# Kernel optimization log

Measured on AMD Instinct MI355X. Metric: run time of the kernel, lower is better.

## Reference

```python
import jax, jax.numpy as jnp
import numpy as np
import math

D_MODEL = 1024
N_HEADS = 16
D_FF = 4096
B, T = 2, 2048
EPS = 1e-5


def setup_inputs() -> dict:
    key = jax.random.key(0)
    ks = jax.random.split(key, 8)
    s = 0.02
    return {
        "x": jax.random.normal(ks[0], (B, T, D_MODEL), jnp.float32),
        "wq": jax.random.normal(ks[1], (D_MODEL, D_MODEL), jnp.float32) * s,
        "wk": jax.random.normal(ks[2], (D_MODEL, D_MODEL), jnp.float32) * s,
        "wv": jax.random.normal(ks[3], (D_MODEL, D_MODEL), jnp.float32) * s,
        "wo": jax.random.normal(ks[4], (D_MODEL, D_MODEL), jnp.float32) * s,
        "ln1_w": jnp.ones((D_MODEL,), jnp.float32),
        "ln2_w": jnp.ones((D_MODEL,), jnp.float32),
        "w1": jax.random.normal(ks[5], (D_FF, D_MODEL), jnp.float32) * s,
        "w2": jax.random.normal(ks[6], (D_MODEL, D_FF), jnp.float32) * s,
    }


def rmsnorm(x, w):
    # weight * x / sqrt(mean(x^2) + eps)
    denom = jnp.sqrt(jnp.mean(jnp.square(x), axis=-1, keepdims=True) + EPS)
    return w * x / denom


def mhsa(x, wq, wk, wv, wo):
    b, t, d = x.shape
    dk = d // N_HEADS
    # Linear(weight shape (out,in)): y = x @ W.T
    q = (x @ wq.T).reshape(b, t, N_HEADS, dk).transpose(0, 2, 1, 3)  # bhtd
    k = (x @ wk.T).reshape(b, t, N_HEADS, dk).transpose(0, 2, 1, 3)
    v = (x @ wv.T).reshape(b, t, N_HEADS, dk).transpose(0, 2, 1, 3)
    scores = jnp.einsum("bhqd,bhkd->bhqk", q, k) / math.sqrt(dk)
    causal = jnp.tril(jnp.ones((t, t), bool))  # True = keep
    scores = jnp.where(causal, scores, -jnp.inf)
    probs = jax.nn.softmax(scores, axis=-1)
    out = jnp.einsum("bhqk,bhkd->bhqd", probs, v)
    out = out.transpose(0, 2, 1, 3).reshape(b, t, d)
    return out @ wo.T


def ffn(x, w1, w2):
    h = jax.nn.gelu(x @ w1.T, approximate=False)  # exact erf GELU
    return h @ w2.T


def reference(x, wq, wk, wv, wo, ln1_w, ln2_w, w1, w2):
    x = x + mhsa(rmsnorm(x, ln1_w), wq, wk, wv, wo)
    x = x + ffn(rmsnorm(x, ln2_w), w1, w2)
    return x
```

## Files before the change

### kernel.cpp

```cpp
#include <hip/hip_runtime.h>
#include <stdint.h>

#define D_MODEL 1024
#define N_HEADS 16
#define D_FF    4096
#define BATCH   2
#define SEQ     2048
#define EPSV    1e-5f
#define MTOK    (BATCH*SEQ)
#define QKVS    3072


typedef __bf16 bf16x8 __attribute__((ext_vector_type(8)));
typedef float  f32x4  __attribute__((ext_vector_type(4)));

#define MFMA_BF16(a,b,c) __builtin_amdgcn_mfma_f32_16x16x32_bf16((a),(b),(c),0,0,0)

__device__ __forceinline__ float b2f(unsigned short u) {
  union { unsigned int i; float f; } c; c.i = ((unsigned int)u) << 16; return c.f;
}
__device__ __forceinline__ unsigned short f2b(float f) {
  union { float f; unsigned int i; } c; c.f = f;
  unsigned int x = c.i;
  unsigned int r = (x + 0x7fffu + ((x >> 16) & 1u)) >> 16;
  return (unsigned short)r;
}
__device__ __forceinline__ unsigned short f2b_trunc(float f) {
  union { float f; unsigned int i; } c; c.f = f;
  return (unsigned short)(c.i >> 16);
}

__device__ __forceinline__ void glds16(const unsigned short* g, unsigned short* l) {
  __builtin_amdgcn_global_load_lds(
      (const __attribute__((address_space(1))) void*)g,
      (__attribute__((address_space(3))) void*)l, 16, 0, 0);
}

__global__ void detect_kernel(const unsigned int* __restrict__ ln1, int* __restrict__ flag) {
  if (threadIdx.x == 0 && blockIdx.x == 0)
    *flag = (ln1[0] == 0x3F800000u) ? 1 : 0;
}

__global__ void convert_all_kernel(
    const void* __restrict__ wq, const void* __restrict__ wk,
    const void* __restrict__ wv, const void* __restrict__ wo,
    const void* __restrict__ w1, const void* __restrict__ w2,
    const void* __restrict__ l1, const void* __restrict__ l2,
    unsigned short* dq, unsigned short* dk, unsigned short* dv, unsigned short* dwo,
    unsigned short* d1, unsigned short* d2, unsigned short* dl1, unsigned short* dl2,
    const int* __restrict__ flag) {
  const int i = blockIdx.x * 256 + threadIdx.x;
  const void* src; unsigned short* dst; int off;
  if (i < 1048576) {
    const int t = i >> 18;  off = i & 262143;
    src = (t == 0) ? wq : (t == 1) ? wk : (t == 2) ? wv : wo;
    dst = (t == 0) ? dq : (t == 1) ? dk : (t == 2) ? dv : dwo;
  } else if (i < 2097152) { off = i - 1048576; src = w1; dst = d1; }
  else if (i < 3145728)   { off = i - 2097152; src = w2; dst = d2; }
  else if (i < 3145984)   { off = i - 3145728; src = l1; dst = dl1; }
  else                    { off = i - 3145984; src = l2; dst = dl2; }
  if (*flag) {
    const float4 v = ((const float4*)src)[off];
    ushort4 o; o.x = f2b(v.x); o.y = f2b(v.y); o.z = f2b(v.z); o.w = f2b(v.w);
    ((ushort4*)dst)[off] = o;
  } else {
    ((ushort4*)dst)[off] = ((const ushort4*)src)[off];
  }
}

__global__ void rmsnorm_kernel(const void* __restrict__ xin,
                               const unsigned short* __restrict__ w,
                               unsigned short* __restrict__ out,
                               const int* __restrict__ f32flag) {
  __shared__ float red[4];
  const int row = blockIdx.x;
  const int tid = threadIdx.x;
  const int base = tid * 4;
  const bool f32 = f32flag && (*f32flag != 0);
  float v0, v1, v2, v3;
  if (f32) {
    const float4 p = ((const float4*)xin)[(size_t)row * 256 + tid];
    v0 = p.x; v1 = p.y; v2 = p.z; v3 = p.w;
  } else {
    const short4 p = *(const short4*)((const unsigned short*)xin + (size_t)row * D_MODEL + base);
    v0 = b2f((unsigned short)p.x); v1 = b2f((unsigned short)p.y);
    v2 = b2f((unsigned short)p.z); v3 = b2f((unsigned short)p.w);
  }
  float ss = v0*v0 + v1*v1 + v2*v2 + v3*v3;
  #pragma unroll
  for (int d = 1; d < 64; d <<= 1) ss += __shfl_xor(ss, d);
  if ((tid & 63) == 0) red[tid >> 6] = ss;
  __syncthreads();
  const float tot = red[0] + red[1] + red[2] + red[3];
  const float inv = 1.0f / sqrtf(tot * (1.0f / (float)D_MODEL) + EPSV);
  short4 ov;
  ov.x = (short)f2b(b2f(w[base + 0]) * v0 * inv);
  ov.y = (short)f2b(b2f(w[base + 1]) * v1 * inv);
  ov.z = (short)f2b(b2f(w[base + 2]) * v2 * inv);
  ov.w = (short)f2b(b2f(w[base + 3]) * v3 * inv);
  *(short4*)(out + (size_t)row * D_MODEL + base) = ov;
}

#define BM 128
#define BK 32
template<int TBN>
__global__ __launch_bounds__(256) void gemm_bt_kernel(
    const unsigned short* __restrict__ A,
    const unsigned short* __restrict__ Bw,
    void* __restrict__ C,
    const void* __restrict__ R,
    int M, int N, int K, int flags,
    const int* __restrict__ outf32_flag,
    const int* __restrict__ resf32_flag) {
  constexpr int JN = TBN / 32;
  constexpr int GA = BM * 4;
  constexpr int GT = (BM + TBN) * 4;
  __shared__ __align__(16) unsigned short As[BM * BK];
  __shared__ __align__(16) unsigned short Bs[TBN * BK];

  const int tid  = threadIdx.x;
  const int w    = tid >> 6, ln = tid & 63;
  const int wm   = w >> 1,  wn = w & 1;
  const int lm   = ln & 15, quad = ln >> 4;

  const int gx = gridDim.x;
  const int L  = blockIdx.x + gx * blockIdx.y;
  const int per = (gx * gridDim.y) >> 3;
  const int tile = (L & 7) * per + (L >> 3);
  const int tileM = (tile / gx) * BM;
  const int tileN = (tile % gx) * TBN;

  f32x4 acc[4][JN];
  #pragma unroll
  for (int i = 0; i < 4; i++)
    #pragma unroll
    for (int j = 0; j < JN; j++) acc[i][j] = (f32x4){0.f, 0.f, 0.f, 0.f};

  for (int k0 = 0; k0 < K; k0 += BK) {
    __syncthreads();
    #pragma unroll
    for (int g0 = 0; g0 < GT; g0 += 256) {
      const int g = g0 + tid;
      if (g0 + 256 <= GA || g < GA) {
        const int r  = g >> 2;
        const int sg = (g & 3) ^ ((g >> 3) & 3);
        glds16(&A[(size_t)(tileM + r) * K + k0 + sg * 8], &As[g * 8]);
      } else {
        const int gb = g - GA;
        const int r  = gb >> 2;
        const int sg = (gb & 3) ^ ((gb >> 3) & 3);
        glds16(&Bw[(size_t)(tileN + r) * K + k0 + sg * 8], &Bs[gb * 8]);
      }
    }
    __syncthreads();

    bf16x8 af[4], bfr[JN];
    #pragma unroll
    for (int i = 0; i < 4; i++) {
      const int r = wm * 64 + i * 16 + lm;
      af[i] = *(const bf16x8*)&As[r * BK + (quad ^ ((r >> 1) & 3)) * 8];
    }
    #pragma unroll
    for (int j = 0; j < JN; j++) {
      const int r = wn * (TBN / 2) + j * 16 + lm;
      bfr[j] = *(const bf16x8*)&Bs[r * BK + (quad ^ ((r >> 1) & 3)) * 8];
    }
    #pragma unroll
    for (int i = 0; i < 4; i++)
      #pragma unroll
      for (int j = 0; j < JN; j++)
        acc[i][j] = MFMA_BF16(af[i], bfr[j], acc[i][j]);
  }

  const bool hasR   = flags & 2;
  const bool dogelu = flags & 8;
  const bool outf32 = outf32_flag && (*outf32_flag != 0);
  const bool rf32   = resf32_flag && (*resf32_flag != 0);
  #pragma unroll
  for (int i = 0; i < 4; i++) {
    #pragma unroll
    for (int j = 0; j < JN; j++) {
      #pragma unroll
      for (int r = 0; r < 4; r++) {
        const int row = tileM + wm * 64 + i * 16 + quad * 4 + r;
        const int col = tileN + wn * (TBN / 2) + j * 16 + lm;
        float val = acc[i][j][r];
        if (dogelu) {
          const float u = 0.7978845608f * (val + 0.044715f * val * val * val);
          const float e = exp2f(u * 2.885390082f);
          val = 0.5f * val * (2.0f - 2.0f / (e + 1.0f));
        }
        const size_t idx = (size_t)row * N + col;
        if (hasR) val += rf32 ? ((const float*)R)[idx]
                              : b2f(((const unsigned short*)R)[idx]);
        if (outf32) ((float*)C)[idx] = val;
        else        ((unsigned short*)C)[idx] = f2b(val);
      }
    }
  }
}

__global__ __launch_bounds__(256) void attn_kernel(
    const unsigned short* __restrict__ QKV,
    unsigned short* __restrict__ O) {
  __shared__ __align__(16) unsigned short Ks [2][64 * 64];
  __shared__ __align__(16) unsigned short VTs[2][64 * 64];
  __shared__ __align__(16) unsigned short Ps [4][16 * 64];

  const int tid = threadIdx.x;
  const int w = tid >> 6, ln = tid & 63;
  const int lm = ln & 15, quad = ln >> 4;
  const f32x4 zf = (f32x4){0.f, 0.f, 0.f, 0.f};

  const int L   = blockIdx.x;
  const int xcd = L & 7;
  const int idx = L >> 3;
  const int bh  = xcd * 4 + (idx >> 4);
  const int pr  = idx & 15;
  const int b   = bh >> 4, h = bh & 15;
  const int qtA = pr, qtB = 31 - pr;
  const int nA = qtA + 1, total = nA + qtB + 1;

  const unsigned short* Qp = QKV + (size_t)b * SEQ * QKVS + h * 64;
  const unsigned short* Kp = Qp + 1024;
  const unsigned short* Vp = Qp + 2048;

  auto scale8 = [](bf16x8 v) -> bf16x8 {
    union { bf16x8 h; unsigned short u[8]; } in, out;
    in.h = v;
    #pragma unroll
    for (int ii = 0; ii < 8; ii++) out.u[ii] = f2b(b2f(in.u[ii]) * 0.1803368801f);
    return out.h;
  };

  bf16x8 qfA0, qfA1, qfB0, qfB1;
  {
    const size_t ra = (size_t)(qtA * 64 + w * 16 + lm) * QKVS;
    qfA0 = scale8(*(const bf16x8*)&Qp[ra + quad * 8]);
    qfA1 = scale8(*(const bf16x8*)&Qp[ra + 32 + quad * 8]);
    const size_t rb = (size_t)(qtB * 64 + w * 16 + lm) * QKVS;
    qfB0 = scale8(*(const bf16x8*)&Qp[rb + quad * 8]);
    qfB1 = scale8(*(const bf16x8*)&Qp[rb + 32 + quad * 8]);
  }

  const int vkey2 = (tid >> 3) << 1;
  const int vd8   = (tid & 7) << 3;
  const int ve    = tid & 7;

  f32x4 oacc[4];
  float lrow[4];
  #pragma unroll
  for (int i = 0; i < 4; i++) oacc[i] = zf;
  #pragma unroll
  for (int r = 0; r < 4; r++) lrow[r] = 0.f;

  union V8 { uint4 u; unsigned short s[8]; };
  V8 v0r, v1r;

  auto issue_stage = [&](int c, int buf) {
    #pragma unroll
    for (int ii = 0; ii < 2; ii++) {
      const int g   = tid + 256 * ii;
      const int key = g >> 3;
      const int sg  = (g & 7) ^ (key & 7);
      glds16(&Kp[(size_t)(c * 64 + key) * QKVS + sg * 8], &Ks[buf][g * 8]);
    }
    v0r.u = *(const uint4*)&Vp[(size_t)(c * 64 + vkey2)     * QKVS + vd8];
    v1r.u = *(const uint4*)&Vp[(size_t)(c * 64 + vkey2 + 1) * QKVS + vd8];
  };

  auto write_vt = [&](int buf) {
    const int swb = (vkey2 >> 3) ^ ve;
    #pragma unroll
    for (int ii = 0; ii < 8; ii++) {
      const int phys = (vd8 + ii) * 64 + swb * 8 + (vkey2 & 7);
      const unsigned int pk = (unsigned int)v0r.s[ii] | ((unsigned int)v1r.s[ii] << 16);
      *(unsigned int*)&VTs[buf][phys] = pk;
    }
  };

  auto write_o = [&](int qt) {
    #pragma unroll
    for (int r = 0; r < 4; r++) {
      float l = lrow[r];
      #pragma unroll
      for (int d2 = 1; d2 < 16; d2 <<= 1) l += __shfl_xor(l, d2);
      const float invl = 1.0f / l;
      const size_t orow = (size_t)(b * SEQ + qt * 64 + w * 16 + quad * 4 + r) * D_MODEL + h * 64;
      #pragma unroll
      for (int nt = 0; nt < 4; nt++)
        O[orow + nt * 16 + lm] = f2b(oacc[nt][r] * invl);
    }
  };

  issue_stage(0, 0);
  for (int j = 0; j < total; j++) {
    const int buf = j & 1;
    write_vt(buf);
    __syncthreads();

    if (j + 1 < total) {
      const int cn = (j + 1 < nA) ? (j + 1) : (j + 1 - nA);
      issue_stage(cn, buf ^ 1);
    }
    if (j == nA) {
      write_o(qtA);
      #pragma unroll
      for (int i = 0; i < 4; i++) oacc[i] = zf;
      #pragma unroll
      for (int r = 0; r < 4; r++) lrow[r] = 0.f;
    }

    const bool isA = j < nA;
    const int  c   = isA ? j : j - nA;
    const int  qt  = isA ? qtA : qtB;
    const bool diag = (c == qt);
    const bf16x8 qf0 = isA ? qfA0 : qfB0;
    const bf16x8 qf1 = isA ? qfA1 : qfB1;

    f32x4 s[4];
    #pragma unroll
    for (int kg = 0; kg < 4; kg++) {
      const int kbase = (kg * 16 + lm) * 64;
      const int s0 = quad ^ (lm & 7);
      const bf16x8 kf0 = *(const bf16x8*)&Ks[buf][kbase + s0 * 8];
      const bf16x8 kf1 = *(const bf16x8*)&Ks[buf][kbase + (s0 ^ 4) * 8];
      s[kg] = MFMA_BF16(qf0, kf0, zf);
      s[kg] = MFMA_BF16(qf1, kf1, s[kg]);
    }

    #pragma unroll
    for (int r = 0; r < 4; r++) {
      float a0 = s[0][r], a1 = s[1][r], a2 = s[2][r], a3 = s[3][r];
      if (diag) {
        const int qloc = w * 16 + quad * 4 + r;
        if (lm      > qloc) a0 = -1e30f;
        if (lm + 16 > qloc) a1 = -1e30f;
        if (lm + 32 > qloc) a2 = -1e30f;
        if (lm + 48 > qloc) a3 = -1e30f;
      }
      const float p0 = exp2f(a0), p1 = exp2f(a1);
      const float p2 = exp2f(a2), p3 = exp2f(a3);
      lrow[r] += (p0 + p1) + (p2 + p3);
      const int row = quad * 4 + r;
      const int rb  = row * 64, r7 = row & 7, lhi = lm >> 3, llo = lm & 7;
      Ps[w][rb + (((0 + lhi) ^ r7) << 3) + llo] = f2b_trunc(p0);
      Ps[w][rb + (((2 + lhi) ^ r7) << 3) + llo] = f2b_trunc(p1);
      Ps[w][rb + (((4 + lhi) ^ r7) << 3) + llo] = f2b_trunc(p2);
      Ps[w][rb + (((6 + lhi) ^ r7) << 3) + llo] = f2b_trunc(p3);
    }

    #pragma unroll
    for (int hh = 0; hh < 2; hh++) {
      const bf16x8 pf = *(const bf16x8*)&Ps[w][lm * 64 + (((hh * 4 + quad) ^ (lm & 7)) << 3)];
      #pragma unroll
      for (int nt = 0; nt < 4; nt++) {
        const int dim = nt * 16 + lm;
        const int swb = (hh * 4 + quad) ^ (dim >> 3);
        const bf16x8 vf = *(const bf16x8*)&VTs[buf][dim * 64 + swb * 8];
        oacc[nt] = MFMA_BF16(pf, vf, oacc[nt]);
      }
    }
  }
  write_o(qtB);
}

extern "C" void kernel_launch(void* const* d_in, const int* in_sizes, int n_in,
                              void* d_out, int out_size, void* d_ws, size_t ws_size,
                              hipStream_t stream) {
  char* ws = (char*)d_ws;
  const size_t MB = 1u << 20;
  unsigned short* cwq  = (unsigned short*)(ws + 8  * MB);
  unsigned short* cwk  = (unsigned short*)(ws + 10 * MB);
  unsigned short* cwv  = (unsigned short*)(ws + 12 * MB);
  unsigned short* cwo  = (unsigned short*)(ws + 14 * MB);
  unsigned short* cln1 = (unsigned short*)(ws + 16 * MB);
  unsigned short* cln2 = (unsigned short*)(ws + 16 * MB + 4096);
  unsigned short* cw1  = (unsigned short*)(ws + 17 * MB);
  unsigned short* cw2  = (unsigned short*)(ws + 25 * MB);
  unsigned short* xn1  = (unsigned short*)(ws + 33 * MB);
  unsigned short* qkv  = (unsigned short*)(ws + 41 * MB);
  unsigned short* y1   = (unsigned short*)(ws + 65 * MB);
  unsigned short* xn2  = (unsigned short*)(ws + 0);
  unsigned short* hbf  = (unsigned short*)(ws + 33 * MB);
  int*            flag = (int*)           (ws + 73 * MB);
  unsigned short* ao   = xn1;

  detect_kernel<<<1, 64, 0, stream>>>((const unsigned int*)d_in[5], flag);

  convert_all_kernel<<<12290, 256, 0, stream>>>(
      d_in[1], d_in[2], d_in[3], d_in[4], d_in[7], d_in[8], d_in[5], d_in[6],
      cwq, cwk, cwv, cwo, cw1, cw2, cln1, cln2, flag);

  rmsnorm_kernel<<<MTOK, 256, 0, stream>>>(d_in[0], cln1, xn1, flag);
  {
    const dim3 g(QKVS / 128, MTOK / BM);
    gemm_bt_kernel<128><<<g, 256, 0, stream>>>(xn1, cwq, qkv, nullptr,
                                               MTOK, QKVS, D_MODEL, 0, nullptr, nullptr);
  }
  attn_kernel<<<512, 256, 0, stream>>>(qkv, ao);
  {
    const dim3 g(D_MODEL / 64, MTOK / BM);
    gemm_bt_kernel<64><<<g, 256, 0, stream>>>(ao, cwo, y1, d_in[0],
                                              MTOK, D_MODEL, D_MODEL, 2, nullptr, flag);
  }
  rmsnorm_kernel<<<MTOK, 256, 0, stream>>>(y1, cln2, xn2, nullptr);
  {
    const dim3 g(D_FF / 128, MTOK / BM);
    gemm_bt_kernel<128><<<g, 256, 0, stream>>>(xn2, cw1, hbf, nullptr,
                                               MTOK, D_FF, D_MODEL, 8, nullptr, nullptr);
  }
  {
    const dim3 g(D_MODEL / 64, MTOK / BM);
    gemm_bt_kernel<64><<<g, 256, 0, stream>>>(hbf, cw2, d_out, y1,
                                              MTOK, D_MODEL, D_FF, 2, flag, nullptr);
  }
}
```

Before: 402.3 us.

## Split K across two warp groups in narrow GEMMs with LDS reduction

```diff
diff --git a/kernel.cpp b/kernel.cpp
--- a/kernel.cpp
+++ b/kernel.cpp
@@ -103,8 +103,8 @@
 
 #define BM 128
 #define BK 32
-template<int TBN>
-__global__ __launch_bounds__(256) void gemm_bt_kernel(
+template<int TBN, int KSEG>
+__global__ __launch_bounds__(256 * KSEG) void gemm_bt_kernel(
     const unsigned short* __restrict__ A,
     const unsigned short* __restrict__ Bw,
     void* __restrict__ C,
@@ -115,13 +115,19 @@
   constexpr int JN = TBN / 32;
   constexpr int GA = BM * 4;
   constexpr int GT = (BM + TBN) * 4;
-  __shared__ __align__(16) unsigned short As[BM * BK];
-  __shared__ __align__(16) unsigned short Bs[TBN * BK];
-
-  const int tid  = threadIdx.x;
-  const int w    = tid >> 6, ln = tid & 63;
-  const int wm   = w >> 1,  wn = w & 1;
-  const int lm   = ln & 15, quad = ln >> 4;
+  __shared__ __align__(16) unsigned short smem[KSEG * (BM + TBN) * BK];
+  unsigned short* Asb = smem;
+  unsigned short* Bsb = smem + KSEG * BM * BK;
+
+  const int tid   = threadIdx.x;
+  const int tid_l = tid & 255;
+  const int w     = tid >> 6;
+  const int kseg  = (KSEG == 1) ? 0 : (w >> 2);
+  const int wm    = (w >> 1) & 1, wn = w & 1;
+  const int ln    = tid & 63;
+  const int lm    = ln & 15, quad = ln >> 4;
+  unsigned short* As = Asb + kseg * BM * BK;
+  unsigned short* Bs = Bsb + kseg * TBN * BK;
 
   const int gx = gridDim.x;
   const int L  = blockIdx.x + gx * blockIdx.y;
@@ -130,26 +136,28 @@
   const int tileM = (tile / gx) * BM;
   const int tileN = (tile % gx) * TBN;
 
+  const int kofs = kseg * (K / KSEG);
+
   f32x4 acc[4][JN];
   #pragma unroll
   for (int i = 0; i < 4; i++)
     #pragma unroll
     for (int j = 0; j < JN; j++) acc[i][j] = (f32x4){0.f, 0.f, 0.f, 0.f};
 
-  for (int k0 = 0; k0 < K; k0 += BK) {
+  for (int k0 = 0; k0 < K / KSEG; k0 += BK) {
     __syncthreads();
     #pragma unroll
     for (int g0 = 0; g0 < GT; g0 += 256) {
-      const int g = g0 + tid;
+      const int g = g0 + tid_l;
       if (g0 + 256 <= GA || g < GA) {
         const int r  = g >> 2;
         const int sg = (g & 3) ^ ((g >> 3) & 3);
-        glds16(&A[(size_t)(tileM + r) * K + k0 + sg * 8], &As[g * 8]);
+        glds16(&A[(size_t)(tileM + r) * K + kofs + k0 + sg * 8], &As[g * 8]);
       } else {
         const int gb = g - GA;
         const int r  = gb >> 2;
         const int sg = (gb & 3) ^ ((gb >> 3) & 3);
-        glds16(&Bw[(size_t)(tileN + r) * K + k0 + sg * 8], &Bs[gb * 8]);
+        glds16(&Bw[(size_t)(tileN + r) * K + kofs + k0 + sg * 8], &Bs[gb * 8]);
       }
     }
     __syncthreads();
@@ -172,29 +180,54 @@
         acc[i][j] = MFMA_BF16(af[i], bfr[j], acc[i][j]);
   }
 
-  const bool hasR   = flags & 2;
-  const bool dogelu = flags & 8;
-  const bool outf32 = outf32_flag && (*outf32_flag != 0);
-  const bool rf32   = resf32_flag && (*resf32_flag != 0);
-  #pragma unroll
-  for (int i = 0; i < 4; i++) {
+  if constexpr (KSEG == 2) {
+    float* scratch = (float*)smem;
     #pragma unroll
     for (int j = 0; j < JN; j++) {
-      #pragma unroll
-      for (int r = 0; r < 4; r++) {
-        const int row = tileM + wm * 64 + i * 16 + quad * 4 + r;
-        const int col = tileN + wn * (TBN / 2) + j * 16 + lm;
-        float val = acc[i][j][r];
-        if (dogelu) {
-          const float u = 0.7978845608f * (val + 0.044715f * val * val * val);
-          const float e = exp2f(u * 2.885390082f);
-          val = 0.5f * val * (2.0f - 2.0f / (e + 1.0f));
+      __syncthreads();
+      if (kseg == 1) {
+        #pragma unroll
+        for (int i = 0; i < 4; i++)
+          #pragma unroll
+          for (int r = 0; r < 4; r++)
+            scratch[tid_l * 16 + i * 4 + r] = acc[i][j][r];
+      }
+      __syncthreads();
+      if (kseg == 0) {
+        #pragma unroll
+        for (int i = 0; i < 4; i++)
+          #pragma unroll
+          for (int r = 0; r < 4; r++)
+            acc[i][j][r] += scratch[tid_l * 16 + i * 4 + r];
+      }
+    }
+  }
+
+  if (kseg == 0) {
+    const bool hasR   = flags & 2;
+    const bool dogelu = flags & 8;
+    const bool outf32 = outf32_flag && (*outf32_flag != 0);
+    const bool rf32   = resf32_flag && (*resf32_flag != 0);
+    #pragma unroll
+    for (int i = 0; i < 4; i++) {
+      #pragma unroll
+      for (int j = 0; j < JN; j++) {
+        #pragma unroll
+        for (int r = 0; r < 4; r++) {
+          const int row = tileM + wm * 64 + i * 16 + quad * 4 + r;
+          const int col = tileN + wn * (TBN / 2) + j * 16 + lm;
+          float val = acc[i][j][r];
+          if (dogelu) {
+            const float u = 0.7978845608f * (val + 0.044715f * val * val * val);
+            const float e = exp2f(u * 2.885390082f);
+            val = 0.5f * val * (2.0f - 2.0f / (e + 1.0f));
+          }
+          const size_t idx = (size_t)row * N + col;
+          if (hasR) val += rf32 ? ((const float*)R)[idx]
+                                : b2f(((const unsigned short*)R)[idx]);
+          if (outf32) ((float*)C)[idx] = val;
+          else        ((unsigned short*)C)[idx] = f2b(val);
         }
-        const size_t idx = (size_t)row * N + col;
-        if (hasR) val += rf32 ? ((const float*)R)[idx]
-                              : b2f(((const unsigned short*)R)[idx]);
-        if (outf32) ((float*)C)[idx] = val;
-        else        ((unsigned short*)C)[idx] = f2b(val);
       }
     }
   }
@@ -395,24 +428,24 @@
   rmsnorm_kernel<<<MTOK, 256, 0, stream>>>(d_in[0], cln1, xn1, flag);
   {
     const dim3 g(QKVS / 128, MTOK / BM);
-    gemm_bt_kernel<128><<<g, 256, 0, stream>>>(xn1, cwq, qkv, nullptr,
-                                               MTOK, QKVS, D_MODEL, 0, nullptr, nullptr);
+    gemm_bt_kernel<128,1><<<g, 256, 0, stream>>>(xn1, cwq, qkv, nullptr,
+                                                 MTOK, QKVS, D_MODEL, 0, nullptr, nullptr);
   }
   attn_kernel<<<512, 256, 0, stream>>>(qkv, ao);
   {
     const dim3 g(D_MODEL / 64, MTOK / BM);
-    gemm_bt_kernel<64><<<g, 256, 0, stream>>>(ao, cwo, y1, d_in[0],
-                                              MTOK, D_MODEL, D_MODEL, 2, nullptr, flag);
+    gemm_bt_kernel<64,2><<<g, 512, 0, stream>>>(ao, cwo, y1, d_in[0],
+                                                MTOK, D_MODEL, D_MODEL, 2, nullptr, flag);
   }
   rmsnorm_kernel<<<MTOK, 256, 0, stream>>>(y1, cln2, xn2, nullptr);
   {
     const dim3 g(D_FF / 128, MTOK / BM);
-    gemm_bt_kernel<128><<<g, 256, 0, stream>>>(xn2, cw1, hbf, nullptr,
-                                               MTOK, D_FF, D_MODEL, 8, nullptr, nullptr);
+    gemm_bt_kernel<128,1><<<g, 256, 0, stream>>>(xn2, cw1, hbf, nullptr,
+                                                 MTOK, D_FF, D_MODEL, 8, nullptr, nullptr);
   }
   {
     const dim3 g(D_MODEL / 64, MTOK / BM);
-    gemm_bt_kernel<64><<<g, 256, 0, stream>>>(hbf, cw2, d_out, y1,
-                                              MTOK, D_MODEL, D_FF, 2, flag, nullptr);
-  }
-}
+    gemm_bt_kernel<64,2><<<g, 512, 0, stream>>>(hbf, cw2, d_out, y1,
+                                                MTOK, D_MODEL, D_FF, 2, flag, nullptr);
+  }
+}
```

After: 392.4 us. 1.03x faster.
